# Kernel tuning notes

Measured on AMD Instinct MI355X. Metric: run time of the kernel, lower is better.

Reference implementation:

```python
import jax, jax.numpy as jnp
import numpy as np

EMBED_DIM = 512
N_HEADS = 8
HEAD_DIM = EMBED_DIM // N_HEADS
B, N = 4, 2048


def setup_inputs() -> dict:
    key = jax.random.key(0)
    ks = jax.random.split(key, 5)
    x = jax.random.normal(ks[0], (B, N, EMBED_DIM), dtype=jnp.float32)
    # torch Linear weights are (out, in); init scale ~ 1/sqrt(in)
    s = 1.0 / np.sqrt(EMBED_DIM)
    WQ = jax.random.uniform(ks[1], (EMBED_DIM, EMBED_DIM), jnp.float32, -s, s)
    WK = jax.random.uniform(ks[2], (EMBED_DIM, EMBED_DIM), jnp.float32, -s, s)
    WV = jax.random.uniform(ks[3], (EMBED_DIM, EMBED_DIM), jnp.float32, -s, s)
    WO = jax.random.uniform(ks[4], (EMBED_DIM, EMBED_DIM), jnp.float32, -s, s)
    mask = jnp.tril(jnp.ones((N, N), dtype=jnp.int32))  # causal mask
    return {"x": x, "WQ": WQ, "WK": WK, "WV": WV, "WO": WO, "mask": mask}


def reference(x, WQ, WK, WV, WO, mask):
    scale = HEAD_DIM ** -0.5
    # Linear: y = x @ W.T ; then split heads -> (B, H, N, Dh)
    def proj(W):
        y = jnp.einsum('bnd,ed->bne', x, W)
        return y.reshape(B, N, N_HEADS, HEAD_DIM).transpose(0, 2, 1, 3)
    Q, K, V = proj(WQ), proj(WK), proj(WV)
    scores = jnp.einsum('bhnd,bhmd->bhnm', Q, K) * scale  # (B,H,N,N)
    scores = jnp.where(mask[None, None, :, :] == 0, -jnp.inf, scores)
    attn = jax.nn.softmax(scores, axis=-1)
    # dropout is identity in eval mode
    out = jnp.einsum('bhnm,bhmd->bhnd', attn, V)
    out = out.transpose(0, 2, 1, 3).reshape(B, N, EMBED_DIM)
    return jnp.einsum('bne,de->bnd', out, WO)
```

## Files before the change

### kernel.cpp

```cpp
#include <hip/hip_runtime.h>
#include <hip/hip_bf16.h>

#define B_  4
#define N_  2048
#define E_  512
#define H_  8
#define DH_ 64
#define M_  (B_ * N_)

typedef __attribute__((ext_vector_type(8))) short bq8;
typedef __attribute__((ext_vector_type(4))) float f32x4;

#define QSCALE_ (0.125f * 1.44269504f)

static __device__ __forceinline__ unsigned short f2bf(float f) {
    unsigned u = __float_as_uint(f);
    unsigned r = (u + 0x7fffu + ((u >> 16) & 1u)) >> 16;
    return (unsigned short)r;
}

static __device__ __forceinline__ unsigned cvtpk_bf16(float lo, float hi) {
    unsigned r;
    asm("v_cvt_pk_bf16_f32 %0, %1, %2" : "=v"(r) : "v"(lo), "v"(hi));
    return r;
}

static __device__ __forceinline__ void gld_lds16(const unsigned short* g,
                                                 unsigned short* l)
{
    __builtin_amdgcn_global_load_lds(
        (const __attribute__((address_space(1))) void*)g,
        (__attribute__((address_space(3))) void*)l,
        16, 0, 0);
}

static __device__ __forceinline__ void cvt16(const void* src, unsigned short* dst,
                                             int base, bool isBf)
{
    if (isBf) {
        const uint4* s = (const uint4*)((const unsigned short*)src + base);
        uint4 a = s[0], b = s[1];
        *(uint4*)(dst + base)     = a;
        *(uint4*)(dst + base + 8) = b;
    } else {
        const float* s = (const float*)src + base;
        unsigned short tmp[16];
        #pragma unroll
        for (int c = 0; c < 16; c += 4) {
            const float4 v = *(const float4*)(s + c);
            tmp[c + 0] = f2bf(v.x); tmp[c + 1] = f2bf(v.y);
            tmp[c + 2] = f2bf(v.z); tmp[c + 3] = f2bf(v.w);
        }
        *(uint4*)(dst + base)     = *(uint4*)&tmp[0];
        *(uint4*)(dst + base + 8) = *(uint4*)&tmp[8];
    }
}

__global__ __launch_bounds__(256)
void cvt_all(const void* __restrict__ sx,
             const void* __restrict__ s0, const void* __restrict__ s1,
             const void* __restrict__ s2, const void* __restrict__ s3,
             unsigned short* __restrict__ dx,
             unsigned short* __restrict__ d0, unsigned short* __restrict__ d1,
             unsigned short* __restrict__ d2, unsigned short* __restrict__ d3,
             int* __restrict__ dflag)
{
    __shared__ int wtot[4];
    const int bid = blockIdx.x;
    const int t   = threadIdx.x;
    const void* s;
    unsigned short* d;
    int base;
    if (bid < 1024) {
        s = sx; d = dx;
        base = bid * 4096 + t * 16;
    } else {
        const int wb = bid - 1024;
        const int wi = wb >> 6;
        s = (wi == 0) ? s0 : (wi == 1) ? s1 : (wi == 2) ? s2 : s3;
        d = (wi == 0) ? d0 : (wi == 1) ? d1 : (wi == 2) ? d2 : d3;
        base = (wb & 63) * 4096 + t * 16;
    }

    const unsigned* sw = (const unsigned*)s;
    int cnt = 0;
    #pragma unroll
    for (int i = 0; i < 4; ++i) {
        const unsigned w = sw[t * 4 + i];
        const unsigned elo = (w >> 7) & 0xffu;
        const unsigned ehi = (w >> 23) & 0xffu;
        cnt += (elo >= 100u && elo <= 150u && ehi >= 100u && ehi <= 150u) ? 1 : 0;
    }
    cnt += __shfl_xor(cnt, 1);  cnt += __shfl_xor(cnt, 2);
    cnt += __shfl_xor(cnt, 4);  cnt += __shfl_xor(cnt, 8);
    cnt += __shfl_xor(cnt, 16); cnt += __shfl_xor(cnt, 32);
    if ((t & 63) == 0) wtot[t >> 6] = cnt;
    __syncthreads();
    const int total = wtot[0] + wtot[1] + wtot[2] + wtot[3];
    const bool isBf = (total >= 512);
    if (bid == 0 && t == 0) dflag[0] = isBf ? 1 : 0;

    cvt16(s, d, base, isBf);
}

template<int BN>
__global__ __launch_bounds__(256)
void gemm_bf16(const unsigned short* __restrict__ A,
               const unsigned short* __restrict__ W0,
               const unsigned short* __restrict__ W1,
               const unsigned short* __restrict__ W2,
               void* __restrict__ C0, void* __restrict__ C1, void* __restrict__ C2,
               const int* __restrict__ dflag, int cSel)
{
    constexpr int NB = BN / 32;
    __shared__ unsigned short As[2][128 * 32];
    __shared__ unsigned short Bs[2][BN * 32];

    const int extBf = dflag[0];
    const unsigned short* Wv = (blockIdx.z == 0) ? W0 : (blockIdx.z == 1) ? W1 : W2;
    void*                 Cv = (blockIdx.z == 0) ? C0 : (blockIdx.z == 1) ? C1 : C2;
    const int  mode  = (cSel == 1) ? 1 : ((blockIdx.z == 2) ? 2 : 0);
    const bool vswap = (mode == 2);
    const float qs = (cSel == 0 && blockIdx.z == 0) ? QSCALE_ : 1.0f;

    const int t    = threadIdx.x;
    const int w    = t >> 6;
    const int lane = t & 63;
    const int ln   = lane & 15;
    const int qd   = lane >> 4;
    const int wm   = w >> 1;
    const int wn   = w & 1;

    const int m0 = blockIdx.x * 128;
    const int n0 = blockIdx.y * BN;

    const int lr = lane >> 2;
    const int lc = (lane & 3) * 8;
    const unsigned short* gA0 = A + (size_t)(m0 + w * 32 + lr) * E_ + lc;
    const unsigned short* gA1 = gA0 + 16 * E_;
    const int aOff0 = w * 32 * 32;
    const int aOff1 = aOff0 + 16 * 32;

    const unsigned short* gB0;
    const unsigned short* gB1 = nullptr;
    int bOff0, bOff1 = 0;
    if (BN == 128) {
        gB0 = Wv + (size_t)(n0 + w * 32 + lr) * E_ + lc;
        gB1 = gB0 + 16 * E_;
        bOff0 = w * 32 * 32;
        bOff1 = bOff0 + 16 * 32;
    } else {
        gB0 = Wv + (size_t)(n0 + w * 16 + lr) * E_ + lc;
        bOff0 = w * 16 * 32;
    }

    f32x4 acc[4][4];
    #pragma unroll
    for (int i = 0; i < 4; ++i)
        #pragma unroll
        for (int j = 0; j < 4; ++j)
            acc[i][j] = (f32x4){0.f, 0.f, 0.f, 0.f};

    for (int k0 = 0; k0 < E_; k0 += 64) {
        __syncthreads();
        gld_lds16(gA0 + k0,      &As[0][aOff0]);
        gld_lds16(gA1 + k0,      &As[0][aOff1]);
        gld_lds16(gA0 + k0 + 32, &As[1][aOff0]);
        gld_lds16(gA1 + k0 + 32, &As[1][aOff1]);
        gld_lds16(gB0 + k0,      &Bs[0][bOff0]);
        gld_lds16(gB0 + k0 + 32, &Bs[1][bOff0]);
        if (BN == 128) {
            gld_lds16(gB1 + k0,      &Bs[0][bOff1]);
            gld_lds16(gB1 + k0 + 32, &Bs[1][bOff1]);
        }
        __syncthreads();

        #pragma unroll
        for (int half = 0; half < 2; ++half) {
            bq8 afr[4], bfr[NB];
            #pragma unroll
            for (int i = 0; i < 4; ++i)
                afr[i] = *(const bq8*)&As[half][(wm * 64 + i * 16 + ln) * 32 + qd * 8];
            #pragma unroll
            for (int j = 0; j < NB; ++j)
                bfr[j] = *(const bq8*)&Bs[half][(wn * (BN / 2) + j * 16 + ln) * 32 + qd * 8];

            if (vswap) {
                #pragma unroll
                for (int i = 0; i < 4; ++i)
                    #pragma unroll
                    for (int j = 0; j < NB; ++j)
                        acc[i][j] = __builtin_amdgcn_mfma_f32_16x16x32_bf16(afr[i], bfr[j], acc[i][j], 0, 0, 0);
            } else {
                #pragma unroll
                for (int i = 0; i < NB; ++i)
                    #pragma unroll
                    for (int j = 0; j < 4; ++j)
                        acc[i][j] = __builtin_amdgcn_mfma_f32_16x16x32_bf16(bfr[i], afr[j], acc[i][j], 0, 0, 0);
            }
        }
    }

    if (mode == 2) {
        unsigned short* C = (unsigned short*)Cv;
        const int colBase = n0 + wn * 64;
        const int hh = colBase >> 6;
        #pragma unroll
        for (int i = 0; i < 4; ++i) {
            const int token = m0 + wm * 64 + i * 16 + qd * 4;
            const int bb = token >> 11;
            const int nn = token & 2047;
            #pragma unroll
            for (int j = 0; j < 4; ++j) {
                const int d = j * 16 + ln;
                ushort4 o4;
                o4.x = f2bf(acc[i][j][0]);
                o4.y = f2bf(acc[i][j][1]);
                o4.z = f2bf(acc[i][j][2]);
                o4.w = f2bf(acc[i][j][3]);
                *(ushort4*)(C + ((size_t)(bb * H_ + hh) * 64 + d) * N_ + nn) = o4;
            }
        }
    } else if (mode == 0 || extBf) {
        unsigned short* C = (unsigned short*)Cv;
        #pragma unroll
        for (int i = 0; i < NB; ++i) {
            const int n = n0 + wn * (BN / 2) + i * 16 + qd * 4;
            #pragma unroll
            for (int j = 0; j < 4; ++j) {
                const int m = m0 + wm * 64 + j * 16 + ln;
                ushort4 o4;
                o4.x = f2bf(acc[i][j][0] * qs);
                o4.y = f2bf(acc[i][j][1] * qs);
                o4.z = f2bf(acc[i][j][2] * qs);
                o4.w = f2bf(acc[i][j][3] * qs);
                *(ushort4*)(C + (size_t)m * E_ + n) = o4;
            }
        }
    } else {
        float* C = (float*)Cv;
        #pragma unroll
        for (int i = 0; i < NB; ++i) {
            const int n = n0 + wn * (BN / 2) + i * 16 + qd * 4;
            #pragma unroll
            for (int j = 0; j < 4; ++j) {
                const int m = m0 + wm * 64 + j * 16 + ln;
                *(f32x4*)(C + (size_t)m * E_ + n) = acc[i][j];
            }
        }
    }
}

__global__ __launch_bounds__(256)
void attn_causal(const unsigned short* __restrict__ Q,
                 const unsigned short* __restrict__ K,
                 const unsigned short* __restrict__ VtG,
                 unsigned short* __restrict__ O)
{
    __shared__ unsigned short Ks[128 * 72];
    __shared__ unsigned short Vs[64 * 136];
    __shared__ unsigned short Pq[64 * 136];

    const int id  = blockIdx.x;
    const int i   = 15 - (id >> 5);
    const int hb  = id & 31;
    const int h   = hb & 7;
    const int b   = hb >> 3;
    const int qlo = 2 * i;
    const int qhi = 2 * i + 1;
    const int CC  = i + 1;

    const int t   = threadIdx.x;
    const int w    = t >> 6;
    const int lane = t & 63;
    const int ln   = lane & 15;
    const int qd   = lane >> 4;

    const int col0 = h * DH_;
    const size_t rowBase = (size_t)b * N_;
    const unsigned short* Vhead = VtG + (size_t)(b * H_ + h) * 64 * N_;

    const int jbase = qd * 4;
    const int mloc  = w * 16 + ln;
    const int qAg = qlo * 64 + mloc;
    const int qBg = qhi * 64 + mloc;
    const int prow = mloc * 136;

    const unsigned short* Qa = Q + (rowBase + qAg) * E_ + col0 + qd * 8;
    const unsigned short* Qb = Q + (rowBase + qBg) * E_ + col0 + qd * 8;
    const bq8 qfA0 = *(const bq8*)(Qa);
    const bq8 qfA1 = *(const bq8*)(Qa + 32);
    const bq8 qfB0 = *(const bq8*)(Qb);
    const bq8 qfB1 = *(const bq8*)(Qb + 32);

    const int kr = t >> 1;
    const int kc = (t & 1) * 32;
    const int vr = t >> 2;
    const int vc = (t & 3) * 32;
    const unsigned short* gK = K + (rowBase + kr) * E_ + col0 + kc;
    const unsigned short* gV = Vhead + (size_t)vr * N_ + vc;

    float lA = 0.f, lB = 0.f;
    f32x4 oA[4], oB[4];
    #pragma unroll
    for (int dt = 0; dt < 4; ++dt) {
        oA[dt] = (f32x4){0.f, 0.f, 0.f, 0.f};
        oB[dt] = (f32x4){0.f, 0.f, 0.f, 0.f};
    }

    uint4 kR0, kR1, kR2, kR3, vR0, vR1, vR2, vR3;
    {
        const uint4* ks = (const uint4*)gK;
        kR0 = ks[0]; kR1 = ks[1]; kR2 = ks[2]; kR3 = ks[3];
        const uint4* vs = (const uint4*)gV;
        vR0 = vs[0]; vR1 = vs[1]; vR2 = vs[2]; vR3 = vs[3];
    }

    for (int kt = 0; kt < CC; ++kt) {
        __syncthreads();
        *(uint4*)&Ks[kr * 72 + kc]      = kR0;
        *(uint4*)&Ks[kr * 72 + kc + 8]  = kR1;
        *(uint4*)&Ks[kr * 72 + kc + 16] = kR2;
        *(uint4*)&Ks[kr * 72 + kc + 24] = kR3;
        *(uint4*)&Vs[vr * 136 + vc]      = vR0;
        *(uint4*)&Vs[vr * 136 + vc + 8]  = vR1;
        *(uint4*)&Vs[vr * 136 + vc + 16] = vR2;
        *(uint4*)&Vs[vr * 136 + vc + 24] = vR3;
        __syncthreads();

        if (kt + 1 < CC) {
            const uint4* ks = (const uint4*)(gK + (size_t)(kt + 1) * 128 * E_);
            kR0 = ks[0]; kR1 = ks[1]; kR2 = ks[2]; kR3 = ks[3];
            const uint4* vs = (const uint4*)(gV + (kt + 1) * 128);
            vR0 = vs[0]; vR1 = vs[1]; vR2 = vs[2]; vR3 = vs[3];
        }

        const int gb = kt * 128 + jbase;
        const bool diag = (kt == CC - 1);

        f32x4 sB[8];
        #pragma unroll
        for (int ct = 0; ct < 8; ++ct) {
            const bq8 kf0 = *(const bq8*)&Ks[(ct * 16 + ln) * 72 + qd * 8];
            const bq8 kf1 = *(const bq8*)&Ks[(ct * 16 + ln) * 72 + 32 + qd * 8];
            __builtin_amdgcn_s_setprio(1);
            f32x4 ca = (f32x4){0.f, 0.f, 0.f, 0.f};
            ca = __builtin_amdgcn_mfma_f32_16x16x32_bf16(kf0, qfA0, ca, 0, 0, 0);
            ca = __builtin_amdgcn_mfma_f32_16x16x32_bf16(kf1, qfA1, ca, 0, 0, 0);
            f32x4 c = (f32x4){0.f, 0.f, 0.f, 0.f};
            c = __builtin_amdgcn_mfma_f32_16x16x32_bf16(kf0, qfB0, c, 0, 0, 0);
            c = __builtin_amdgcn_mfma_f32_16x16x32_bf16(kf1, qfB1, c, 0, 0, 0);
            __builtin_amdgcn_s_setprio(0);
            sB[ct] = c;
            float p0 = exp2f(ca[0]);
            float p1 = exp2f(ca[1]);
            float p2 = exp2f(ca[2]);
            float p3 = exp2f(ca[3]);
            if (diag) {
                const int kb = gb + ct * 16;
                if (kb + 0 > qAg) p0 = 0.f;
                if (kb + 1 > qAg) p1 = 0.f;
                if (kb + 2 > qAg) p2 = 0.f;
                if (kb + 3 > qAg) p3 = 0.f;
            }
            lA += (p0 + p1) + (p2 + p3);
            uint2 pk2;
            pk2.x = cvtpk_bf16(p0, p1);
            pk2.y = cvtpk_bf16(p2, p3);
            *(uint2*)&Pq[prow + ct * 16 + jbase] = pk2;
        }
        const bq8 pA0 = *(const bq8*)&Pq[prow + qd * 8];
        const bq8 pA1 = *(const bq8*)&Pq[prow + 32 + qd * 8];
        const bq8 pA2 = *(const bq8*)&Pq[prow + 64 + qd * 8];
        const bq8 pA3 = *(const bq8*)&Pq[prow + 96 + qd * 8];

        #pragma unroll
        for (int ct = 0; ct < 8; ++ct) {
            float p0 = exp2f(sB[ct][0]);
            float p1 = exp2f(sB[ct][1]);
            float p2 = exp2f(sB[ct][2]);
            float p3 = exp2f(sB[ct][3]);
            if (diag) {
                const int kb = gb + ct * 16;
                if (kb + 0 > qBg) p0 = 0.f;
                if (kb + 1 > qBg) p1 = 0.f;
                if (kb + 2 > qBg) p2 = 0.f;
                if (kb + 3 > qBg) p3 = 0.f;
            }
            lB += (p0 + p1) + (p2 + p3);
            uint2 pk2;
            pk2.x = cvtpk_bf16(p0, p1);
            pk2.y = cvtpk_bf16(p2, p3);
            *(uint2*)&Pq[prow + ct * 16 + jbase] = pk2;
        }
        const bq8 pB0 = *(const bq8*)&Pq[prow + qd * 8];
        const bq8 pB1 = *(const bq8*)&Pq[prow + 32 + qd * 8];
        const bq8 pB2 = *(const bq8*)&Pq[prow + 64 + qd * 8];
        const bq8 pB3 = *(const bq8*)&Pq[prow + 96 + qd * 8];

        __builtin_amdgcn_s_setprio(1);
        #pragma unroll
        for (int dt = 0; dt < 4; ++dt) {
            const int vb = (dt * 16 + ln) * 136;
            const bq8 vf0 = *(const bq8*)&Vs[vb + qd * 8];
            const bq8 vf1 = *(const bq8*)&Vs[vb + 32 + qd * 8];
            const bq8 vf2 = *(const bq8*)&Vs[vb + 64 + qd * 8];
            const bq8 vf3 = *(const bq8*)&Vs[vb + 96 + qd * 8];
            oB[dt] = __builtin_amdgcn_mfma_f32_16x16x32_bf16(vf0, pB0, oB[dt], 0, 0, 0);
            oB[dt] = __builtin_amdgcn_mfma_f32_16x16x32_bf16(vf1, pB1, oB[dt], 0, 0, 0);
            oB[dt] = __builtin_amdgcn_mfma_f32_16x16x32_bf16(vf2, pB2, oB[dt], 0, 0, 0);
            oB[dt] = __builtin_amdgcn_mfma_f32_16x16x32_bf16(vf3, pB3, oB[dt], 0, 0, 0);
            oA[dt] = __builtin_amdgcn_mfma_f32_16x16x32_bf16(vf0, pA0, oA[dt], 0, 0, 0);
            oA[dt] = __builtin_amdgcn_mfma_f32_16x16x32_bf16(vf1, pA1, oA[dt], 0, 0, 0);
            oA[dt] = __builtin_amdgcn_mfma_f32_16x16x32_bf16(vf2, pA2, oA[dt], 0, 0, 0);
            oA[dt] = __builtin_amdgcn_mfma_f32_16x16x32_bf16(vf3, pA3, oA[dt], 0, 0, 0);
        }
        __builtin_amdgcn_s_setprio(0);
    }

    lA += __shfl_xor(lA, 16); lA += __shfl_xor(lA, 32);
    lB += __shfl_xor(lB, 16); lB += __shfl_xor(lB, 32);
    const float invA = 1.f / lA;
    const float invB = 1.f / lB;

    unsigned short* oAp = O + (rowBase + qlo * 64 + mloc) * E_ + col0 + jbase;
    unsigned short* oBp = O + (rowBase + qhi * 64 + mloc) * E_ + col0 + jbase;
    #pragma unroll
    for (int dt = 0; dt < 4; ++dt) {
        uint2 a2, b2;
        a2.x = cvtpk_bf16(oA[dt][0] * invA, oA[dt][1] * invA);
        a2.y = cvtpk_bf16(oA[dt][2] * invA, oA[dt][3] * invA);
        b2.x = cvtpk_bf16(oB[dt][0] * invB, oB[dt][1] * invB);
        b2.y = cvtpk_bf16(oB[dt][2] * invB, oB[dt][3] * invB);
        *(uint2*)(oAp + dt * 16) = a2;
        *(uint2*)(oBp + dt * 16) = b2;
    }
}

extern "C" void kernel_launch(void* const* d_in, const int* in_sizes, int n_in,
                              void* d_out, int out_size, void* d_ws, size_t ws_size,
                              hipStream_t stream)
{
    const void* x  = d_in[0];
    const void* WQ = d_in[1];
    const void* WK = d_in[2];
    const void* WV = d_in[3];
    const void* WO = d_in[4];

    int* dflag = (int*)d_ws;
    unsigned short* xb  = (unsigned short*)((char*)d_ws + 256);
    unsigned short* wqb = xb  + (size_t)M_ * E_;
    unsigned short* wkb = wqb + (size_t)E_ * E_;
    unsigned short* wvb = wkb + (size_t)E_ * E_;
    unsigned short* wob = wvb + (size_t)E_ * E_;
    unsigned short* q   = wob + (size_t)E_ * E_;
    unsigned short* k   = q   + (size_t)M_ * E_;
    unsigned short* v   = k   + (size_t)M_ * E_;
    unsigned short* o   = v   + (size_t)M_ * E_;

    cvt_all<<<1280, 256, 0, stream>>>(x, WQ, WK, WV, WO,
                                      xb, wqb, wkb, wvb, wob, dflag);

    gemm_bf16<128><<<dim3(M_ / 128, E_ / 128, 3), 256, 0, stream>>>(
        xb, wqb, wkb, wvb, q, k, v, dflag, 0);

    attn_causal<<<512, 256, 0, stream>>>(q, k, v, o);

    gemm_bf16<64><<<dim3(M_ / 128, E_ / 64, 1), 256, 0, stream>>>(
        o, wob, wob, wob, d_out, d_out, d_out, dflag, 1);
}
```

Measured before the change: 171.7 us.

## Split long causal attention rows across two blocks with a combine pass

The heavy query tiles (i>=8) have their KV loop split in two halves, each handled by a separate block that writes unnormalised bf16 partial outputs and row sums to a workspace reusing the xb buffer. A new combine kernel adds the partials and normalises them. A reordered schedule table interleaves split and unsplit work to balance load across the 768 blocks. This relies on the softmax using a fixed (non-running) max, so partials can be summed directly. It costs an extra launch and partial-buffer traffic, and the partials are rounded to bf16 before they are combined.

After: 175.2 us. 2.0% more time.

```diff
diff --git a/kernel.cpp b/kernel.cpp
--- a/kernel.cpp
+++ b/kernel.cpp
@@ -17,6 +17,9 @@
     unsigned u = __float_as_uint(f);
     unsigned r = (u + 0x7fffu + ((u >> 16) & 1u)) >> 16;
     return (unsigned short)r;
+}
+static __device__ __forceinline__ float bf2f(unsigned short u) {
+    return __uint_as_float(((unsigned)u) << 16);
 }
 
 static __device__ __forceinline__ unsigned cvtpk_bf16(float lo, float hi) {
@@ -251,24 +254,36 @@
     }
 }
 
+static __device__ const signed char TAB_I[24] =
+    {15,15,14, 7,14,13,13,12, 6,12,11,11,10, 5,10, 9, 9, 8, 4, 8, 3, 2, 1, 0};
+static __device__ const signed char TAB_S[24] =
+    { 0, 1, 1,-1, 0, 0, 1, 1,-1, 0, 0, 1, 1,-1, 0, 0, 1, 1,-1, 0,-1,-1,-1,-1};
+
+#define PBYTES_ 16896
+
 __global__ __launch_bounds__(256)
 void attn_causal(const unsigned short* __restrict__ Q,
                  const unsigned short* __restrict__ K,
                  const unsigned short* __restrict__ VtG,
-                 unsigned short* __restrict__ O)
+                 unsigned short* __restrict__ O,
+                 void* __restrict__ Part)
 {
     __shared__ unsigned short Ks[128 * 72];
     __shared__ unsigned short Vs[64 * 136];
     __shared__ unsigned short Pq[64 * 136];
 
-    const int id  = blockIdx.x;
-    const int i   = 15 - (id >> 5);
-    const int hb  = id & 31;
+    const int ord = blockIdx.x >> 5;
+    const int hb  = blockIdx.x & 31;
+    const int i   = TAB_I[ord];
+    const int sS  = TAB_S[ord];
     const int h   = hb & 7;
     const int b   = hb >> 3;
     const int qlo = 2 * i;
     const int qhi = 2 * i + 1;
     const int CC  = i + 1;
+    const int half = CC >> 1;
+    const int kt0 = (sS == 1) ? half : 0;
+    const int ktE = (sS == 0) ? half : CC;
 
     const int t   = threadIdx.x;
     const int w    = t >> 6;
@@ -310,13 +325,13 @@
 
     uint4 kR0, kR1, kR2, kR3, vR0, vR1, vR2, vR3;
     {
-        const uint4* ks = (const uint4*)gK;
+        const uint4* ks = (const uint4*)(gK + (size_t)kt0 * 128 * E_);
         kR0 = ks[0]; kR1 = ks[1]; kR2 = ks[2]; kR3 = ks[3];
-        const uint4* vs = (const uint4*)gV;
+        const uint4* vs = (const uint4*)(gV + kt0 * 128);
         vR0 = vs[0]; vR1 = vs[1]; vR2 = vs[2]; vR3 = vs[3];
     }
 
-    for (int kt = 0; kt < CC; ++kt) {
+    for (int kt = kt0; kt < ktE; ++kt) {
         __syncthreads();
         *(uint4*)&Ks[kr * 72 + kc]      = kR0;
         *(uint4*)&Ks[kr * 72 + kc + 8]  = kR1;
@@ -328,7 +343,7 @@
         *(uint4*)&Vs[vr * 136 + vc + 24] = vR3;
         __syncthreads();
 
-        if (kt + 1 < CC) {
+        if (kt + 1 < ktE) {
             const uint4* ks = (const uint4*)(gK + (size_t)(kt + 1) * 128 * E_);
             kR0 = ks[0]; kR1 = ks[1]; kR2 = ks[2]; kR3 = ks[3];
             const uint4* vs = (const uint4*)(gV + (kt + 1) * 128);
@@ -420,20 +435,79 @@
 
     lA += __shfl_xor(lA, 16); lA += __shfl_xor(lA, 32);
     lB += __shfl_xor(lB, 16); lB += __shfl_xor(lB, 32);
-    const float invA = 1.f / lA;
-    const float invB = 1.f / lB;
-
-    unsigned short* oAp = O + (rowBase + qlo * 64 + mloc) * E_ + col0 + jbase;
-    unsigned short* oBp = O + (rowBase + qhi * 64 + mloc) * E_ + col0 + jbase;
+
+    if (sS >= 0) {
+        char* slotBase = (char*)Part
+                       + (size_t)(((i - 8) * 32 + hb) * 2 + sS) * PBYTES_;
+        unsigned short* Po = (unsigned short*)slotBase;
+        float*          Pl = (float*)(slotBase + 16384);
+        unsigned short* pa = Po + mloc * 64 + jbase;
+        unsigned short* pb = Po + (64 + mloc) * 64 + jbase;
+        #pragma unroll
+        for (int dt = 0; dt < 4; ++dt) {
+            uint2 a2, b2;
+            a2.x = cvtpk_bf16(oA[dt][0], oA[dt][1]);
+            a2.y = cvtpk_bf16(oA[dt][2], oA[dt][3]);
+            b2.x = cvtpk_bf16(oB[dt][0], oB[dt][1]);
+            b2.y = cvtpk_bf16(oB[dt][2], oB[dt][3]);
+            *(uint2*)(pa + dt * 16) = a2;
+            *(uint2*)(pb + dt * 16) = b2;
+        }
+        if (qd == 0) {
+            Pl[mloc]      = lA;
+            Pl[64 + mloc] = lB;
+        }
+    } else {
+        const float invA = 1.f / lA;
+        const float invB = 1.f / lB;
+        unsigned short* oAp = O + (rowBase + qlo * 64 + mloc) * E_ + col0 + jbase;
+        unsigned short* oBp = O + (rowBase + qhi * 64 + mloc) * E_ + col0 + jbase;
+        #pragma unroll
+        for (int dt = 0; dt < 4; ++dt) {
+            uint2 a2, b2;
+            a2.x = cvtpk_bf16(oA[dt][0] * invA, oA[dt][1] * invA);
+            a2.y = cvtpk_bf16(oA[dt][2] * invA, oA[dt][3] * invA);
+            b2.x = cvtpk_bf16(oB[dt][0] * invB, oB[dt][1] * invB);
+            b2.y = cvtpk_bf16(oB[dt][2] * invB, oB[dt][3] * invB);
+            *(uint2*)(oAp + dt * 16) = a2;
+            *(uint2*)(oBp + dt * 16) = b2;
+        }
+    }
+}
+
+__global__ __launch_bounds__(256)
+void attn_combine(const void* __restrict__ Part, unsigned short* __restrict__ O)
+{
+    const int pi = blockIdx.x >> 5;
+    const int hb = blockIdx.x & 31;
+    const int h  = hb & 7;
+    const int b  = hb >> 3;
+    const int i  = pi + 8;
+    const char* s0 = (const char*)Part + (size_t)((pi * 32 + hb) * 2 + 0) * PBYTES_;
+    const char* s1 = s0 + PBYTES_;
+    const unsigned short* o0 = (const unsigned short*)s0;
+    const unsigned short* o1 = (const unsigned short*)s1;
+    const float* l0 = (const float*)(s0 + 16384);
+    const float* l1 = (const float*)(s1 + 16384);
+
+    const int t   = threadIdx.x;
+    const int row = t >> 1;
+    const int d0  = (t & 1) * 32;
+    const float inv = 1.f / (l0[row] + l1[row]);
+    const int q = (row < 64) ? (2 * i * 64 + row) : ((2 * i + 1) * 64 + (row - 64));
+    unsigned short* dst = O + ((size_t)b * N_ + q) * E_ + h * 64 + d0;
+    const unsigned short* a = o0 + row * 64 + d0;
+    const unsigned short* c = o1 + row * 64 + d0;
     #pragma unroll
-    for (int dt = 0; dt < 4; ++dt) {
-        uint2 a2, b2;
-        a2.x = cvtpk_bf16(oA[dt][0] * invA, oA[dt][1] * invA);
-        a2.y = cvtpk_bf16(oA[dt][2] * invA, oA[dt][3] * invA);
-        b2.x = cvtpk_bf16(oB[dt][0] * invB, oB[dt][1] * invB);
-        b2.y = cvtpk_bf16(oB[dt][2] * invB, oB[dt][3] * invB);
-        *(uint2*)(oAp + dt * 16) = a2;
-        *(uint2*)(oBp + dt * 16) = b2;
+    for (int cc = 0; cc < 32; cc += 4) {
+        const ushort4 va = *(const ushort4*)(a + cc);
+        const ushort4 vc = *(const ushort4*)(c + cc);
+        uint2 o2;
+        o2.x = cvtpk_bf16((bf2f(va.x) + bf2f(vc.x)) * inv,
+                          (bf2f(va.y) + bf2f(vc.y)) * inv);
+        o2.y = cvtpk_bf16((bf2f(va.z) + bf2f(vc.z)) * inv,
+                          (bf2f(va.w) + bf2f(vc.w)) * inv);
+        *(uint2*)(dst + cc) = o2;
     }
 }
 
@@ -458,13 +532,16 @@
     unsigned short* v   = k   + (size_t)M_ * E_;
     unsigned short* o   = v   + (size_t)M_ * E_;
 
+    void* part = (void*)xb;
+
     cvt_all<<<1280, 256, 0, stream>>>(x, WQ, WK, WV, WO,
                                       xb, wqb, wkb, wvb, wob, dflag);
 
     gemm_bf16<128><<<dim3(M_ / 128, E_ / 128, 3), 256, 0, stream>>>(
         xb, wqb, wkb, wvb, q, k, v, dflag, 0);
 
-    attn_causal<<<512, 256, 0, stream>>>(q, k, v, o);
+    attn_causal<<<768, 256, 0, stream>>>(q, k, v, o, part);
+    attn_combine<<<256, 256, 0, stream>>>(part, o);
 
     gemm_bf16<64><<<dim3(M_ / 128, E_ / 64, 1), 256, 0, stream>>>(
         o, wob, wob, wob, d_out, d_out, d_out, dflag, 1);
```
